# Optimization experiments

Hardware: AMD Instinct MI355X
Metric: run time of the kernel (lower is better)

The kernel has to match this reference:

```python
import jax, jax.numpy as jnp
import numpy as np

_EPS = 1e-10
_SHIFT = 1  # init kwarg `shift`

R, N = 65536, 192  # rays, samples per ray


def setup_inputs() -> dict:
    key = jax.random.key(0)
    k1, k2, k3 = jax.random.split(key, 3)
    rgbs = jax.random.uniform(k1, (R, N, 3), dtype=jnp.float32)
    densities = jax.random.uniform(k2, (R, N), dtype=jnp.float32)
    points_3d = jax.random.normal(k3, (R, N, 3), dtype=jnp.float32)
    return {"rgbs": rgbs, "densities": densities, "points_3d": points_3d}


def reference(rgbs, densities, points_3d):
    num_ray_points = points_3d.shape[-2]
    pts = points_3d.reshape(-1, num_ray_points, 3)
    # regular sampling: single scalar step size taken from the first ray
    delta = jnp.linalg.norm(pts[0, 1, :] - pts[0, 0, :])
    alpha = 1.0 - jnp.exp(-densities * delta)          # (R, N)
    trans = jnp.cumprod(1.0 - alpha + _EPS, axis=-1)   # transmittance, (R, N)
    trans = jnp.roll(trans, _SHIFT, axis=-1)
    trans = trans.at[..., :_SHIFT].set(1.0)
    weights = trans * alpha                            # (R, N)
    rgbs_rendered = jnp.sum(weights[..., None] * rgbs, axis=-2)  # (R, 3)
    return rgbs_rendered
```

## Files before the change

### kernel.cpp

```cpp
#include <hip/hip_runtime.h>
#include <math.h>


constexpr int N_SAMP = 192;
constexpr float EPS = 1e-10f;

__global__ __launch_bounds__(256) void render_kernel(
    const float* __restrict__ rgbs,
    const float* __restrict__ dens,
    const float* __restrict__ pts,
    float* __restrict__ out,
    int R)
{
    const int lane = threadIdx.x & 63;
    const int ray  = (blockIdx.x * blockDim.x + threadIdx.x) >> 6;
    if (ray >= R) return;

    const float dx = pts[3] - pts[0];
    const float dy = pts[4] - pts[1];
    const float dz = pts[5] - pts[2];
    const float delta = sqrtf(dx * dx + dy * dy + dz * dz);

    const float* __restrict__ dp = dens + (size_t)ray * N_SAMP + 3 * lane;
    const float* __restrict__ rp = rgbs + ((size_t)ray * N_SAMP + 3 * lane) * 3;

    float dv[3];
#pragma unroll
    for (int i = 0; i < 3; ++i) dv[i] = dp[i];

    float r[9];
#pragma unroll
    for (int i = 0; i < 9; ++i) r[i] = rp[i];

    float a[3], t[3];
#pragma unroll
    for (int i = 0; i < 3; ++i) {
        a[i] = 1.0f - __expf(-dv[i] * delta);
        t[i] = 1.0f - a[i] + EPS;
    }

    float incl = t[0] * t[1] * t[2];
#pragma unroll
    for (int off = 1; off < 64; off <<= 1) {
        const float up = __shfl_up(incl, off, 64);
        incl *= (lane >= off) ? up : 1.0f;
    }
    float excl = __shfl_up(incl, 1, 64);
    if (lane == 0) excl = 1.0f;

    const float w0 = excl * a[0];
    const float e1 = excl * t[0];
    const float w1 = e1 * a[1];
    const float w2 = e1 * t[1] * a[2];

    float sr = w0 * r[0] + w1 * r[3] + w2 * r[6];
    float sg = w0 * r[1] + w1 * r[4] + w2 * r[7];
    float sb = w0 * r[2] + w1 * r[5] + w2 * r[8];

#pragma unroll
    for (int off = 32; off >= 1; off >>= 1) {
        sr += __shfl_down(sr, off, 64);
        sg += __shfl_down(sg, off, 64);
        sb += __shfl_down(sb, off, 64);
    }
    if (lane == 0) {
        float* o = out + (size_t)ray * 3;
        o[0] = sr;
        o[1] = sg;
        o[2] = sb;
    }
}

extern "C" void kernel_launch(void* const* d_in, const int* in_sizes, int n_in,
                              void* d_out, int out_size, void* d_ws, size_t ws_size,
                              hipStream_t stream) {
    const float* rgbs = (const float*)d_in[0];
    const float* dens = (const float*)d_in[1];
    const float* pts  = (const float*)d_in[2];
    float* out = (float*)d_out;

    const int R = in_sizes[1] / N_SAMP;

    const int waves_per_block = 4;
    dim3 block(256);
    dim3 grid((R + waves_per_block - 1) / waves_per_block);
    render_kernel<<<grid, block, 0, stream>>>(rgbs, dens, pts, out, R);
}
```

Before: 34.25 us.

## Use persistent grid-stride waves with software-prefetched next-ray loads

The one-wave-per-ray launch becomes a fixed grid of 2048 blocks. Each wave loops over rays with a stride equal to the total wave count and issues the loads for the next ray before computing the current one. The aim is to hide memory latency and cut block launch overhead, at the cost of more registers for the double buffer and possibly fewer resident waves for latency hiding.

```diff
diff --git a/kernel.cpp b/kernel.cpp
--- a/kernel.cpp
+++ b/kernel.cpp
@@ -5,33 +5,21 @@
 constexpr int N_SAMP = 192;
 constexpr float EPS = 1e-10f;
 
-__global__ __launch_bounds__(256) void render_kernel(
-    const float* __restrict__ rgbs,
-    const float* __restrict__ dens,
-    const float* __restrict__ pts,
-    float* __restrict__ out,
-    int R)
-{
-    const int lane = threadIdx.x & 63;
-    const int ray  = (blockIdx.x * blockDim.x + threadIdx.x) >> 6;
-    if (ray >= R) return;
-
-    const float dx = pts[3] - pts[0];
-    const float dy = pts[4] - pts[1];
-    const float dz = pts[5] - pts[2];
-    const float delta = sqrtf(dx * dx + dy * dy + dz * dz);
-
+__device__ __forceinline__ void load_ray(const float* __restrict__ dens,
+                                         const float* __restrict__ rgbs,
+                                         int ray, int lane,
+                                         float dv[3], float r[9]) {
     const float* __restrict__ dp = dens + (size_t)ray * N_SAMP + 3 * lane;
     const float* __restrict__ rp = rgbs + ((size_t)ray * N_SAMP + 3 * lane) * 3;
-
-    float dv[3];
 #pragma unroll
     for (int i = 0; i < 3; ++i) dv[i] = dp[i];
-
-    float r[9];
 #pragma unroll
     for (int i = 0; i < 9; ++i) r[i] = rp[i];
+}
 
+__device__ __forceinline__ void compute_ray(int ray, int lane, float delta,
+                                            const float dv[3], const float r[9],
+                                            float* __restrict__ out) {
     float a[3], t[3];
 #pragma unroll
     for (int i = 0; i < 3; ++i) {
@@ -71,6 +59,42 @@
     }
 }
 
+__global__ __launch_bounds__(256) void render_kernel(
+    const float* __restrict__ rgbs,
+    const float* __restrict__ dens,
+    const float* __restrict__ pts,
+    float* __restrict__ out,
+    int R)
+{
+    const int lane   = threadIdx.x & 63;
+    const int wave   = (blockIdx.x * blockDim.x + threadIdx.x) >> 6;
+    const int nwaves = (gridDim.x * blockDim.x) >> 6;
+
+    const float dx = pts[3] - pts[0];
+    const float dy = pts[4] - pts[1];
+    const float dz = pts[5] - pts[2];
+    const float delta = sqrtf(dx * dx + dy * dy + dz * dz);
+
+    int ray = wave;
+    if (ray >= R) return;
+
+    float dv[3], r[9];
+    load_ray(dens, rgbs, ray, lane, dv, r);
+
+    for (;;) {
+        const int next = ray + nwaves;
+        float dv2[3], r2[9];
+        if (next < R) load_ray(dens, rgbs, next, lane, dv2, r2);
+        compute_ray(ray, lane, delta, dv, r, out);
+        if (next >= R) break;
+#pragma unroll
+        for (int i = 0; i < 3; ++i) dv[i] = dv2[i];
+#pragma unroll
+        for (int i = 0; i < 9; ++i) r[i] = r2[i];
+        ray = next;
+    }
+}
+
 extern "C" void kernel_launch(void* const* d_in, const int* in_sizes, int n_in,
                               void* d_out, int out_size, void* d_ws, size_t ws_size,
                               hipStream_t stream) {
@@ -81,8 +105,9 @@
 
     const int R = in_sizes[1] / N_SAMP;
 
-    const int waves_per_block = 4;
     dim3 block(256);
-    dim3 grid((R + waves_per_block - 1) / waves_per_block);
-    render_kernel<<<grid, block, 0, stream>>>(rgbs, dens, pts, out, R);
+    int nblocks = 2048;
+    const int max_blocks = (R + 3) / 4;
+    if (nblocks > max_blocks) nblocks = max_blocks;
+    render_kernel<<<dim3(nblocks), block, 0, stream>>>(rgbs, dens, pts, out, R);
 }
```

Result: slower. 36.15 us (+5.6%).
